# Optimization experiments

Measured on AMD Instinct MI355X. Metric: run time of the kernel, lower is better.

Reference implementation:

```python
import jax, jax.numpy as jnp
import numpy as np

D_MODEL = 256
HEADS = 4
HEAD_DIM = D_MODEL // HEADS  # 64
BN_EPS = 1e-5


def conv1(x, W, b):
    # Conv1d kernel_size=1 == per-position linear: x [B,C,N], W [O,C], b [O]
    return jnp.einsum('oc,bcn->bon', W, x) + b[:, None]


def setup_inputs() -> dict:
    key = jax.random.key(0)
    ks = jax.random.split(key, 12)
    B, N, M = 4, 4096, 4096
    s = 0.02
    return {
        'x': jax.random.normal(ks[0], (B, D_MODEL, N), jnp.float32),
        'source': jax.random.normal(ks[1], (B, D_MODEL, M), jnp.float32),
        'pq_w': jax.random.normal(ks[2], (D_MODEL, D_MODEL), jnp.float32) * s,
        'pq_b': jnp.zeros((D_MODEL,), jnp.float32),
        'pk_w': jax.random.normal(ks[3], (D_MODEL, D_MODEL), jnp.float32) * s,
        'pk_b': jnp.zeros((D_MODEL,), jnp.float32),
        'pv_w': jax.random.normal(ks[4], (D_MODEL, D_MODEL), jnp.float32) * s,
        'pv_b': jnp.zeros((D_MODEL,), jnp.float32),
        'merge_w': jax.random.normal(ks[5], (D_MODEL, D_MODEL), jnp.float32) * s,
        'merge_b': jnp.zeros((D_MODEL,), jnp.float32),
        'mlp1_w': jax.random.normal(ks[6], (2 * D_MODEL, 2 * D_MODEL), jnp.float32) * s,
        'mlp1_b': jax.random.normal(ks[7], (2 * D_MODEL,), jnp.float32) * s,
        'bn_gamma': jnp.ones((2 * D_MODEL,), jnp.float32),
        'bn_beta': jnp.zeros((2 * D_MODEL,), jnp.float32),
        'mlp2_w': jax.random.normal(ks[8], (D_MODEL, 2 * D_MODEL), jnp.float32) * s,
        'mlp2_b': jnp.zeros((D_MODEL,), jnp.float32),  # nn.init.constant_(mlp[-1].bias, 0.0)
    }


def reference(x, source, pq_w, pq_b, pk_w, pk_b, pv_w, pv_b,
              merge_w, merge_b, mlp1_w, mlp1_b, bn_gamma, bn_beta,
              mlp2_w, mlp2_b):
    B = x.shape[0]
    # projections; torch view(B, dim, heads, -1): channels split as (head_dim, heads)
    q = conv1(x, pq_w, pq_b).reshape(B, HEAD_DIM, HEADS, -1)       # [B,d,h,N]
    k = conv1(source, pk_w, pk_b).reshape(B, HEAD_DIM, HEADS, -1)  # [B,d,h,M]
    v = conv1(source, pv_w, pv_b).reshape(B, HEAD_DIM, HEADS, -1)
    scores = jnp.einsum('bdhn,bdhm->bhnm', q, k) / (HEAD_DIM ** 0.5)
    prob = jax.nn.softmax(scores, axis=-1)                          # [B,h,N,M]
    attn_out = jnp.einsum('bhnm,bdhm->bdhn', prob, v).reshape(B, D_MODEL, -1)
    message = conv1(attn_out, merge_w, merge_b)                     # [B,D,N]
    # MLP: conv(512->512) + BatchNorm1d (training-mode batch stats) + ReLU + conv(512->256)
    h = conv1(jnp.concatenate([x, message], axis=1), mlp1_w, mlp1_b)  # [B,2D,N]
    mean = jnp.mean(h, axis=(0, 2), keepdims=True)
    var = jnp.var(h, axis=(0, 2), keepdims=True)  # biased, as torch BN uses for normalization
    h = bn_gamma[:, None] * (h - mean) * jax.lax.rsqrt(var + BN_EPS) + bn_beta[:, None]
    h = jax.nn.relu(h)
    return conv1(h, mlp2_w, mlp2_b)
```

## Files before the change

kernel.cpp:

```cpp
#include <hip/hip_runtime.h>
#include <hip/hip_bf16.h>

#define D_MODEL 256
#define HEADS 4
#define HD 64
#define BATCH 4
#define SEQ 4096
#define NPOS (BATCH*SEQ)
#define SCALE_LOG2 0.18033688011112042f
#define MCHUNKS 2

typedef __attribute__((ext_vector_type(4))) float floatx4;
typedef __attribute__((ext_vector_type(8))) short bf16x8;
typedef __attribute__((ext_vector_type(4))) short bf16x4;
typedef __attribute__((ext_vector_type(4))) unsigned short ushortx4;

__device__ __forceinline__ float bf2f(unsigned short b) {
    return __uint_as_float(((unsigned int)b) << 16);
}
__device__ __forceinline__ unsigned short f2bf(float f) {
    unsigned int u = __float_as_uint(f);
    return (unsigned short)((u + 0x7fffu + ((u >> 16) & 1u)) >> 16);
}
__device__ __forceinline__ bf16x4 pack_bf16x4(float a, float b, float c, float d) {
    __hip_bfloat162 lo = __float22bfloat162_rn(float2{a, b});
    __hip_bfloat162 hi = __float22bfloat162_rn(float2{c, d});
    union { __hip_bfloat162 h2[2]; bf16x4 v; } u;
    u.h2[0] = lo; u.h2[1] = hi;
    return u.v;
}
__device__ __forceinline__ bf16x8 pack_bf16x8(floatx4 a, floatx4 b) {
    union { bf16x4 h[2]; bf16x8 v; } u;
    u.h[0] = pack_bf16x4(a[0], a[1], a[2], a[3]);
    u.h[1] = pack_bf16x4(b[0], b[1], b[2], b[3]);
    return u.v;
}
#define MFMA(a,b,c) __builtin_amdgcn_mfma_f32_16x16x32_bf16((a),(b),(c),0,0,0)
#define EXP2(x) __builtin_amdgcn_exp2f(x)

__global__ __launch_bounds__(256) void prep(
        const float* __restrict__ pq_w, const float* __restrict__ pk_w,
        const float* __restrict__ pv_w, const float* __restrict__ merge_w,
        const float* __restrict__ mlp1_w, const float* __restrict__ mlp2_w,
        const float* __restrict__ x, const float* __restrict__ src,
        unsigned short* __restrict__ wqb, unsigned short* __restrict__ wkb,
        unsigned short* __restrict__ wvb, unsigned short* __restrict__ wmt,
        unsigned short* __restrict__ w1b, unsigned short* __restrict__ w2b,
        unsigned short* __restrict__ xT, unsigned short* __restrict__ srcT)
{
    __shared__ unsigned short lT[64][264];
    const int t = threadIdx.x;
    const int bx = blockIdx.x;
    if (bx < 576) {
        int linear = bx * 1024 + t * 4;
        const float* srcW; unsigned short* dst; int off;
        if (linear < 65536)       { srcW = pq_w;   dst = wqb; off = 0; }
        else if (linear < 131072) { srcW = pk_w;   dst = wkb; off = 65536; }
        else if (linear < 196608) { srcW = pv_w;   dst = wvb; off = 131072; }
        else if (linear < 458752) { srcW = mlp1_w; dst = w1b; off = 196608; }
        else                      { srcW = mlp2_w; dst = w2b; off = 458752; }
        int i = linear - off;
        float4 w = *(const float4*)&srcW[i];
        ushortx4 s = { f2bf(w.x), f2bf(w.y), f2bf(w.z), f2bf(w.w) };
        *(ushortx4*)&dst[i] = s;
        return;
    }
    if (bx < 640) {
        int i = (bx - 576) * 1024 + t * 4;
        int cp = i >> 8, o = i & 255;
        int pc = ((cp & 63) << 2) | (cp >> 6);
        unsigned short s[4];
#pragma unroll
        for (int j = 0; j < 4; ++j)
            s[j] = f2bf(merge_w[(size_t)(o + j) * 256 + pc]);
        *(ushortx4*)&wmt[i] = *(const ushortx4*)s;
        return;
    }
    int z = bx - 640;
    const float* X = (z < 256) ? x : src;
    unsigned short* O = (z < 256) ? xT : srcT;
    int rem = z & 255;
    int b = rem >> 6, n0 = (rem & 63) * 64;
#pragma unroll
    for (int r = 0; r < 16; ++r) {
        int idx = r * 256 + t;
        int ch = idx >> 4, nnq = (idx & 15) * 4;
        float4 v4 = *(const float4*)&X[((size_t)b * 256 + ch) * SEQ + n0 + nnq];
        lT[nnq + 0][ch] = f2bf(v4.x);
        lT[nnq + 1][ch] = f2bf(v4.y);
        lT[nnq + 2][ch] = f2bf(v4.z);
        lT[nnq + 3][ch] = f2bf(v4.w);
    }
    __syncthreads();
#pragma unroll
    for (int r = 0; r < 8; ++r) {
        int idx = r * 256 + t;
        int row = idx >> 5, cg = (idx & 31) * 8;
        *(bf16x8*)&O[((size_t)b * SEQ + n0 + row) * 256 + cg] = *(const bf16x8*)&lT[row][cg];
    }
}

__global__ __launch_bounds__(256) void prep2(
        const float* __restrict__ mlp1_w, const float* __restrict__ mlp1_b,
        const float* __restrict__ merge_b, const unsigned short* __restrict__ wmt,
        unsigned short* __restrict__ w1f, float* __restrict__ b1f)
{
    __shared__ unsigned short lA[64][40];
    __shared__ unsigned short lB[128][40];
    const int t = threadIdx.x;
    if (blockIdx.y == 8) {
        int o2 = blockIdx.x * 256 + t;
        float s = mlp1_b[o2];
        for (int o = 0; o < 256; ++o)
            s += mlp1_w[(size_t)o2 * 512 + 256 + o] * merge_b[o];
        b1f[o2] = s;
        return;
    }
    const int lane = t & 63, wid = t >> 6;
    const int wm = wid >> 1, wn = wid & 1;
    const int lrow = lane & 15, quad = lane >> 4;
    const int o20 = blockIdx.y * 64;
    const int c0  = blockIdx.x * 128;

    floatx4 acc[2][4];
#pragma unroll
    for (int i = 0; i < 2; ++i)
#pragma unroll
        for (int j = 0; j < 4; ++j) acc[i][j] = (floatx4){0.f,0.f,0.f,0.f};

    for (int k0 = 0; k0 < 256; k0 += 32) {
#pragma unroll
        for (int r = 0; r < 2; ++r) {
            int linear = r * 1024 + t * 4;
            int row = linear >> 5, col = linear & 31;
            float4 w = *(const float4*)&mlp1_w[(size_t)(o20 + row) * 512 + 256 + k0 + col];
            ushortx4 s = { f2bf(w.x), f2bf(w.y), f2bf(w.z), f2bf(w.w) };
            *(ushortx4*)&lA[row][col] = s;
        }
#pragma unroll
        for (int r = 0; r < 2; ++r) {
            int linear = r * 256 + t;
            int row = linear >> 2, cg = (linear & 3) * 8;
            *(bf16x8*)&lB[row][cg] = *(const bf16x8*)&wmt[(size_t)(c0 + row) * 256 + k0 + cg];
        }
        __syncthreads();
        bf16x8 aF[2], bF[4];
        const int kq = quad * 8;
#pragma unroll
        for (int mt = 0; mt < 2; ++mt)
            aF[mt] = *(const bf16x8*)&lA[wm*32 + mt*16 + lrow][kq];
#pragma unroll
        for (int nt = 0; nt < 4; ++nt)
            bF[nt] = *(const bf16x8*)&lB[wn*64 + nt*16 + lrow][kq];
#pragma unroll
        for (int mt = 0; mt < 2; ++mt)
#pragma unroll
            for (int nt = 0; nt < 4; ++nt)
                acc[mt][nt] = MFMA(aF[mt], bF[nt], acc[mt][nt]);
        __syncthreads();
    }
#pragma unroll
    for (int nt = 0; nt < 4; ++nt) {
        int cp = c0 + wn*64 + nt*16 + lrow;
#pragma unroll
        for (int mt = 0; mt < 2; ++mt)
#pragma unroll
            for (int j = 0; j < 4; ++j) {
                int o2 = o20 + wm*32 + mt*16 + quad*4 + j;
                w1f[(size_t)o2 * 256 + cp] = f2bf(acc[mt][nt][j]);
            }
    }
}

__global__ __launch_bounds__(256) void proj_qkv_all(
        const unsigned short* __restrict__ Wq, const float* __restrict__ bq,
        const unsigned short* __restrict__ Wk, const float* __restrict__ bk,
        const unsigned short* __restrict__ Wv, const float* __restrict__ bv,
        const unsigned short* __restrict__ xT, const unsigned short* __restrict__ srcT,
        unsigned short* __restrict__ qo, unsigned short* __restrict__ ko,
        unsigned short* __restrict__ vo)
{
    __shared__ unsigned short smem[128 * 80];
    unsigned short (*lA)[40] = (unsigned short (*)[40])smem;
    unsigned short (*lB)[40] = (unsigned short (*)[40])(smem + 128 * 40);
    unsigned short (*stage)[72] = (unsigned short (*)[72])smem;
    unsigned short* stage2 = smem;
    const int t = threadIdx.x;
    const int lane = t & 63, wid = t >> 6;
    const int wm = wid >> 1, wn = wid & 1;
    const int lrow = lane & 15, quad = lane >> 4;
    const int mode = blockIdx.x >> 1;
    const int ob = (blockIdx.x & 1) * 128;
    const int n0 = blockIdx.y * 128;
    const int b  = blockIdx.z;
    const unsigned short* W  = (mode == 0) ? Wq : (mode == 1) ? Wk : Wv;
    const float* bias        = (mode == 0) ? bq : (mode == 1) ? bk : bv;
    const unsigned short* XT = (mode == 0) ? xT : srcT;
    unsigned short* out      = (mode == 0) ? qo : (mode == 1) ? ko : vo;

    const int srow[2] = { (0*256 + t) >> 2, (1*256 + t) >> 2 };
    const int scg = (t & 3) * 8;

    floatx4 acc[4][4];
#pragma unroll
    for (int i = 0; i < 4; ++i)
#pragma unroll
        for (int j = 0; j < 4; ++j) acc[i][j] = (floatx4){0.f,0.f,0.f,0.f};

    bf16x8 rW[2], rX[2];
#pragma unroll
    for (int r = 0; r < 2; ++r) {
        rW[r] = *(const bf16x8*)&W[(size_t)(ob + srow[r]) * 256 + scg];
        rX[r] = *(const bf16x8*)&XT[((size_t)b * SEQ + n0 + srow[r]) * 256 + scg];
    }
#pragma unroll
    for (int r = 0; r < 2; ++r) {
        *(bf16x8*)&lA[srow[r]][scg] = rW[r];
        *(bf16x8*)&lB[srow[r]][scg] = rX[r];
    }
    __syncthreads();

    for (int kc = 0; kc < 8; ++kc) {
        const bool pre = (kc + 1 < 8);
        if (pre) {
            const int k1 = (kc + 1) * 32;
#pragma unroll
            for (int r = 0; r < 2; ++r) {
                rW[r] = *(const bf16x8*)&W[(size_t)(ob + srow[r]) * 256 + k1 + scg];
                rX[r] = *(const bf16x8*)&XT[((size_t)b * SEQ + n0 + srow[r]) * 256 + k1 + scg];
            }
        }
        bf16x8 aF[4], bF[4];
        const int kq = quad * 8;
#pragma unroll
        for (int mt = 0; mt < 4; ++mt)
            aF[mt] = *(const bf16x8*)&lA[wm*64 + mt*16 + lrow][kq];
#pragma unroll
        for (int nt = 0; nt < 4; ++nt)
            bF[nt] = *(const bf16x8*)&lB[wn*64 + nt*16 + lrow][kq];
#pragma unroll
        for (int mt = 0; mt < 4; ++mt)
#pragma unroll
            for (int nt = 0; nt < 4; ++nt)
                acc[mt][nt] = MFMA(aF[mt], bF[nt], acc[mt][nt]);
        __syncthreads();
        if (pre) {
#pragma unroll
            for (int r = 0; r < 2; ++r) {
                *(bf16x8*)&lA[srow[r]][scg] = rW[r];
                *(bf16x8*)&lB[srow[r]][scg] = rX[r];
            }
            __syncthreads();
        }
    }
    const float osc = (mode == 0) ? SCALE_LOG2 : 1.0f;
    if (mode == 2) {
        for (int half = 0; half < 2; ++half) {
            __syncthreads();
            if (wm == half) {
#pragma unroll
                for (int mt = 0; mt < 4; ++mt)
#pragma unroll
                    for (int j = 0; j < 4; ++j) {
                        int ol = mt*16 + quad*4 + j;
                        float bvv = bias[ob + half*64 + ol];
#pragma unroll
                        for (int nt = 0; nt < 4; ++nt) {
                            int n = wn*64 + nt*16 + lrow;
                            stage2[ol*132 + n] = f2bf(acc[mt][nt][j] + bvv);
                        }
                    }
            }
            __syncthreads();
#pragma unroll
            for (int i = 0; i < 4; ++i) {
                int c = i * 256 + t;
                int row = c >> 4, sub = c & 15;
                int o = ob + half*64 + row;
                int d = o >> 2, h = o & 3;
                *(bf16x8*)&out[((size_t)(b*HEADS + h) * HD + d) * SEQ + n0 + sub*8] =
                    *(const bf16x8*)&stage2[row*132 + sub*8];
            }
        }
        return;
    }
    for (int half = 0; half < 2; ++half) {
        __syncthreads();
        if (wm == half) {
#pragma unroll
            for (int mt = 0; mt < 4; ++mt)
#pragma unroll
                for (int j = 0; j < 4; ++j) {
                    int o = ob + half*64 + mt*16 + quad*4 + j;
                    float bvv = bias[o];
                    int col = j*16 + mt*4 + quad;
#pragma unroll
                    for (int nt = 0; nt < 4; ++nt) {
                        int n = wn*64 + nt*16 + lrow;
                        stage[n][col] = f2bf((acc[mt][nt][j] + bvv) * osc);
                    }
                }
        }
        __syncthreads();
#pragma unroll
        for (int i = 0; i < 4; ++i) {
            int c = i * 256 + t;
            int n = c >> 3, h = (c >> 1) & 3, sub = c & 1;
            bf16x8 val = *(const bf16x8*)&stage[n][h*16 + sub*8];
            int d0 = (ob >> 2) + half*16 + sub*8;
            *(bf16x8*)&out[((size_t)(b*HEADS + h) * SEQ + n0 + n) * HD + d0] = val;
        }
    }
}

__global__ __launch_bounds__(256, 2) void flash_attn(
        const unsigned short* __restrict__ q,
        const unsigned short* __restrict__ k,
        const unsigned short* __restrict__ v,
        unsigned short* __restrict__ poO, float* __restrict__ pol)
{
    __shared__ unsigned short smem[2][9216];
    const int t = threadIdx.x, lane = t & 63, wid = t >> 6;
    const int lrow = lane & 15, quad = lane >> 4;
    const int bc = blockIdx.x, qt = blockIdx.y;
    const int bh = bc & 15, chunk = bc >> 4;
    const int hb = (bh & 3) * BATCH + (bh >> 2);
    const int r0 = qt * 256 + wid * 64;

    bf16x8 qf[4][2];
#pragma unroll
    for (int nh = 0; nh < 4; ++nh) {
        const size_t base = ((size_t)bh * SEQ + r0 + nh*16 + lrow) * HD;
        qf[nh][0] = *(const bf16x8*)&q[base + quad * 8];
        qf[nh][1] = *(const bf16x8*)&q[base + 32 + quad * 8];
    }
    bf16x8 ones;
#pragma unroll
    for (int i = 0; i < 8; ++i) ones[i] = (short)0x3F80;
    int mmv[2], cgv[2], krv[2];
#pragma unroll
    for (int r = 0; r < 2; ++r) {
        int linear = r * 256 + t;
        int mm = linear >> 3, cg = (linear & 7) * 8;
        int c2 = mm >> 5, mp = mm & 31;
        mmv[r] = mm; cgv[r] = cg;
        krv[r] = (c2 << 5) + ((mp & 4) << 2) + ((mp >> 3) << 2) + (mp & 3);
    }
    const size_t kbase = ((size_t)bh * SEQ + chunk * (SEQ/MCHUNKS));
    const size_t vbase = (size_t)bh * HD;
    const int moff = chunk * (SEQ/MCHUNKS);
    const int NIT = SEQ / MCHUNKS / 64;

    floatx4 oacc[4][4], oaccL[4];
#pragma unroll
    for (int nh = 0; nh < 4; ++nh) {
        oaccL[nh] = (floatx4){0.f,0.f,0.f,0.f};
#pragma unroll
        for (int i = 0; i < 4; ++i) oacc[nh][i] = (floatx4){0.f,0.f,0.f,0.f};
    }

    {
        bf16x8 pk[2], pv[2];
#pragma unroll
        for (int r = 0; r < 2; ++r) {
            pk[r] = *(const bf16x8*)&k[(kbase + mmv[r]) * HD + cgv[r]];
            pv[r] = *(const bf16x8*)&v[(vbase + mmv[r]) * SEQ + moff + cgv[r]];
        }
#pragma unroll
        for (int r = 0; r < 2; ++r) {
            *(bf16x8*)&smem[0][krv[r]*72 + cgv[r]]        = pk[r];
            *(bf16x8*)&smem[0][4608 + mmv[r]*72 + cgv[r]] = pv[r];
        }
    }
    __syncthreads();

    int p = 0;
#pragma unroll 1
    for (int it = 0; it < NIT; ++it) {
        bf16x8 pk[2], pv[2];
        const bool pre = (it + 1 < NIT);
        if (pre) {
            const int m1 = (it + 1) * 64;
#pragma unroll
            for (int r = 0; r < 2; ++r) {
                pk[r] = *(const bf16x8*)&k[(kbase + m1 + mmv[r]) * HD + cgv[r]];
                pv[r] = *(const bf16x8*)&v[(vbase + mmv[r]) * SEQ + moff + m1 + cgv[r]];
            }
        }
        const unsigned short* lS = smem[p];

#pragma unroll
        for (int c2 = 0; c2 < 2; ++c2) {
            floatx4 sa[2][4];
#pragma unroll
            for (int AB = 0; AB < 2; ++AB)
#pragma unroll
                for (int nh = 0; nh < 4; ++nh)
                    sa[AB][nh] = (floatx4){0.f,0.f,0.f,0.f};
            __builtin_amdgcn_s_setprio(1);
#pragma unroll
            for (int AB = 0; AB < 2; ++AB) {
#pragma unroll
                for (int kc = 0; kc < 2; ++kc) {
                    bf16x8 kf = *(const bf16x8*)&lS[(c2*32 + AB*16 + lrow)*72 + kc*32 + quad*8];
#pragma unroll
                    for (int nh = 0; nh < 4; ++nh)
                        sa[AB][nh] = MFMA(kf, qf[nh][kc], sa[AB][nh]);
                }
            }
            __builtin_amdgcn_s_setprio(0);
            bf16x8 pf8[4];
#pragma unroll
            for (int nh = 0; nh < 4; ++nh) {
                floatx4 ea, eb;
#pragma unroll
                for (int i = 0; i < 4; ++i) { ea[i] = EXP2(sa[0][nh][i]); eb[i] = EXP2(sa[1][nh][i]); }
                pf8[nh] = pack_bf16x8(ea, eb);
            }
            __builtin_amdgcn_s_setprio(1);
#pragma unroll
            for (int nh = 0; nh < 4; ++nh)
                oaccL[nh] = MFMA(ones, pf8[nh], oaccL[nh]);
#pragma unroll
            for (int dt = 0; dt < 4; ++dt) {
                bf16x8 vf = *(const bf16x8*)&lS[4608 + (dt*16 + lrow)*72 + c2*32 + quad*8];
#pragma unroll
                for (int nh = 0; nh < 4; ++nh)
                    oacc[nh][dt] = MFMA(vf, pf8[nh], oacc[nh][dt]);
            }
            __builtin_amdgcn_s_setprio(0);
        }
        if (pre) {
#pragma unroll
            for (int r = 0; r < 2; ++r) {
                *(bf16x8*)&smem[p^1][krv[r]*72 + cgv[r]]        = pk[r];
                *(bf16x8*)&smem[p^1][4608 + mmv[r]*72 + cgv[r]] = pv[r];
            }
        }
        __syncthreads();
        p ^= 1;
    }
    const size_t prow = (size_t)(chunk*16 + hb) * SEQ + qt * 256;
    if (lane < 16) {
#pragma unroll
        for (int nh = 0; nh < 4; ++nh)
            pol[prow + wid*64 + nh*16 + lrow] = oaccL[nh][0];
    }
    unsigned short* stB = (unsigned short*)&smem[0][0];
#pragma unroll
    for (int nh = 0; nh < 4; ++nh)
#pragma unroll
        for (int dt = 0; dt < 4; ++dt) {
            bf16x4 pv4 = pack_bf16x4(oacc[nh][dt][0], oacc[nh][dt][1],
                                     oacc[nh][dt][2], oacc[nh][dt][3]);
            *(bf16x4*)&stB[(wid*64 + nh*16 + lrow)*72 + dt*16 + quad*4] = pv4;
        }
    __syncthreads();
#pragma unroll
    for (int i = 0; i < 8; ++i) {
        int c = i * 256 + t;
        int row = c >> 3, sub = c & 7;
        *(bf16x8*)&poO[(prow + row) * HD + sub*8] = *(const bf16x8*)&stB[row*72 + sub*8];
    }
}

__global__ __launch_bounds__(256) void gemm_mlp1(
        const unsigned short* __restrict__ xT, const unsigned short* __restrict__ poO,
        const float* __restrict__ pol,
        const unsigned short* __restrict__ w1b, const unsigned short* __restrict__ w1f,
        const float* __restrict__ b1f, unsigned short* __restrict__ h1,
        float* __restrict__ sums, float* __restrict__ sumsq)
{
    __shared__ unsigned short lA[2][64][40];
    __shared__ unsigned short lB[2][128][40];
    __shared__ float sInv[256];
    const int t = threadIdx.x;
    const int lane = t & 63, wid = t >> 6;
    const int wm = wid >> 1, wn = wid & 1;
    const int lrow = lane & 15, quad = lane >> 4;
    const int o0 = blockIdx.x * 128;
    const int p0 = blockIdx.y * 64;
    const int b = p0 >> 12, n0 = p0 & (SEQ - 1);
    const size_t CH = (size_t)16 * SEQ * HD;

    {
        int h = t >> 6, nn = t & 63;
        int hb = h * BATCH + b;
        float l = 0.f;
#pragma unroll
        for (int c = 0; c < MCHUNKS; ++c)
            l += pol[((size_t)(c*16 + hb)) * SEQ + n0 + nn];
        sInv[t] = 1.0f / l;
    }
    __syncthreads();

    const int arow = t >> 2, acg = (t & 3) * 8;
    const int brow[2] = { (0*256 + t) >> 2, (1*256 + t) >> 2 };

    floatx4 acc[2][4];
#pragma unroll
    for (int i = 0; i < 2; ++i)
#pragma unroll
        for (int j = 0; j < 4; ++j) acc[i][j] = (floatx4){0.f,0.f,0.f,0.f};

    bf16x8 rA, rB[2];
    auto load_tile = [&](int k0) {
        if (k0 < 256) {
            rA = *(const bf16x8*)&xT[(size_t)(p0 + arow) * 256 + k0 + acg];
#pragma unroll
            for (int r = 0; r < 2; ++r)
                rB[r] = *(const bf16x8*)&w1b[(size_t)(o0 + brow[r]) * 512 + k0 + acg];
        } else {
            const int kk2 = k0 - 256;
            const int h = kk2 >> 6, d0 = kk2 & 63, hb = h * BATCH + b;
            const unsigned short* bse = &poO[((size_t)hb * SEQ + n0 + arow) * HD + d0 + acg];
            float inv = sInv[h*64 + arow];
            float fs[8];
#pragma unroll
            for (int i = 0; i < 8; ++i) fs[i] = 0.f;
#pragma unroll
            for (int c = 0; c < MCHUNKS; ++c) {
                bf16x8 a = *(const bf16x8*)(bse + (size_t)c * CH);
#pragma unroll
                for (int i = 0; i < 8; ++i)
                    fs[i] += bf2f((unsigned short)a[i]);
            }
            unsigned short res[8];
#pragma unroll
            for (int i = 0; i < 8; ++i)
                res[i] = f2bf(fs[i] * inv);
            rA = *(const bf16x8*)res;
#pragma unroll
            for (int r = 0; r < 2; ++r)
                rB[r] = *(const bf16x8*)&w1f[(size_t)(o0 + brow[r]) * 256 + kk2 + acg];
        }
    };

    load_tile(0);
    *(bf16x8*)&lA[0][arow][acg] = rA;
#pragma unroll
    for (int r = 0; r < 2; ++r) *(bf16x8*)&lB[0][brow[r]][acg] = rB[r];
    __syncthreads();

    int p = 0;
    for (int kc = 0; kc < 16; ++kc) {
        const bool pre = (kc + 1 < 16);
        if (pre) load_tile((kc + 1) * 32);
        bf16x8 aF[2], bF[4];
        const int kq = quad * 8;
#pragma unroll
        for (int mt = 0; mt < 2; ++mt)
            aF[mt] = *(const bf16x8*)&lA[p][wm*32 + mt*16 + lrow][kq];
#pragma unroll
        for (int nt = 0; nt < 4; ++nt)
            bF[nt] = *(const bf16x8*)&lB[p][wn*64 + nt*16 + lrow][kq];
#pragma unroll
        for (int mt = 0; mt < 2; ++mt)
#pragma unroll
            for (int nt = 0; nt < 4; ++nt)
                acc[mt][nt] = MFMA(aF[mt], bF[nt], acc[mt][nt]);
        if (pre) {
            *(bf16x8*)&lA[p^1][arow][acg] = rA;
#pragma unroll
            for (int r = 0; r < 2; ++r) *(bf16x8*)&lB[p^1][brow[r]][acg] = rB[r];
        }
        __syncthreads();
        p ^= 1;
    }
#pragma unroll
    for (int nt = 0; nt < 4; ++nt) {
        int o = o0 + wn*64 + nt*16 + lrow;
        float bvv = b1f[o];
        float s = 0.f, qs = 0.f;
#pragma unroll
        for (int mt = 0; mt < 2; ++mt)
#pragma unroll
            for (int j = 0; j < 4; ++j) {
                int pos = p0 + wm*32 + mt*16 + quad*4 + j;
                float val = acc[mt][nt][j] + bvv;
                h1[(size_t)pos * 512 + o] = f2bf(val);
                s += val; qs += val * val;
            }
        s  += __shfl_xor(s, 16);  s  += __shfl_xor(s, 32);
        qs += __shfl_xor(qs, 16); qs += __shfl_xor(qs, 32);
        if (lane < 16) {
            atomicAdd(&sums[o], s);
            atomicAdd(&sumsq[o], qs);
        }
    }
}

__global__ __launch_bounds__(256) void gemm_mlp2(
        const unsigned short* __restrict__ W2, const unsigned short* __restrict__ h1,
        const float* __restrict__ bias,
        const float* __restrict__ sums, const float* __restrict__ sumsq,
        const float* __restrict__ gamma, const float* __restrict__ beta,
        float* __restrict__ out)
{
    __shared__ unsigned short lA[2][128][40];
    __shared__ unsigned short lB[2][64][40];
    __shared__ float sSc[512], sSh[512];
    const int t = threadIdx.x;
    const int lane = t & 63, wid = t >> 6;
    const int wm = wid >> 1, wn = wid & 1;
    const int lrow = lane & 15, quad = lane >> 4;
    const int o0 = blockIdx.x * 128;
    const int p0 = blockIdx.y * 64;

#pragma unroll
    for (int cc = 0; cc < 2; ++cc) {
        int c = cc * 256 + t;
        float mean = sums[c] * (1.0f / NPOS);
        float var  = sumsq[c] * (1.0f / NPOS) - mean * mean;
        float sc = gamma[c] * rsqrtf(var + 1e-5f);
        sSc[c] = sc;
        sSh[c] = beta[c] - mean * sc;
    }
    __syncthreads();

    const int arow[2] = { (0*256 + t) >> 2, (1*256 + t) >> 2 };
    const int acg = (t & 3) * 8;
    const int brow = t >> 2;

    floatx4 acc[4][2];
#pragma unroll
    for (int i = 0; i < 4; ++i)
#pragma unroll
        for (int j = 0; j < 2; ++j) acc[i][j] = (floatx4){0.f,0.f,0.f,0.f};

    bf16x8 rW[2], rH;
    auto load_tile = [&](int k0) {
#pragma unroll
        for (int r = 0; r < 2; ++r)
            rW[r] = *(const bf16x8*)&W2[(size_t)(o0 + arow[r]) * 512 + k0 + acg];
        bf16x8 hv = *(const bf16x8*)&h1[(size_t)(p0 + brow) * 512 + k0 + acg];
        unsigned short res[8];
#pragma unroll
        for (int i = 0; i < 8; ++i) {
            int c = k0 + acg + i;
            float f = bf2f((unsigned short)hv[i]);
            f = fmaxf(f * sSc[c] + sSh[c], 0.f);
            res[i] = f2bf(f);
        }
        rH = *(const bf16x8*)res;
    };

    load_tile(0);
#pragma unroll
    for (int r = 0; r < 2; ++r) *(bf16x8*)&lA[0][arow[r]][acg] = rW[r];
    *(bf16x8*)&lB[0][brow][acg] = rH;
    __syncthreads();

    int p = 0;
    for (int kc = 0; kc < 16; ++kc) {
        const bool pre = (kc + 1 < 16);
        if (pre) load_tile((kc + 1) * 32);
        bf16x8 aF[4], bF[2];
        const int kq = quad * 8;
#pragma unroll
        for (int mt = 0; mt < 4; ++mt)
            aF[mt] = *(const bf16x8*)&lA[p][wm*64 + mt*16 + lrow][kq];
#pragma unroll
        for (int nt = 0; nt < 2; ++nt)
            bF[nt] = *(const bf16x8*)&lB[p][wn*32 + nt*16 + lrow][kq];
#pragma unroll
        for (int mt = 0; mt < 4; ++mt)
#pragma unroll
            for (int nt = 0; nt < 2; ++nt)
                acc[mt][nt] = MFMA(aF[mt], bF[nt], acc[mt][nt]);
        if (pre) {
#pragma unroll
            for (int r = 0; r < 2; ++r) *(bf16x8*)&lA[p^1][arow[r]][acg] = rW[r];
            *(bf16x8*)&lB[p^1][brow][acg] = rH;
        }
        __syncthreads();
        p ^= 1;
    }
#pragma unroll
    for (int mt = 0; mt < 4; ++mt)
#pragma unroll
        for (int j = 0; j < 4; ++j) {
            int o = o0 + wm*64 + mt*16 + quad*4 + j;
            float bvv = bias[o];
#pragma unroll
            for (int nt = 0; nt < 2; ++nt) {
                int pos = p0 + wn*32 + nt*16 + lrow;
                int b = pos >> 12, n = pos & (SEQ - 1);
                out[((size_t)b * D_MODEL + o) * SEQ + n] = acc[mt][nt][j] + bvv;
            }
        }
}

extern "C" void kernel_launch(void* const* d_in, const int* in_sizes, int n_in,
                              void* d_out, int out_size, void* d_ws, size_t ws_size,
                              hipStream_t stream)
{
    (void)in_sizes; (void)n_in; (void)out_size; (void)ws_size;
    const float* x        = (const float*)d_in[0];
    const float* source   = (const float*)d_in[1];
    const float* pq_w     = (const float*)d_in[2];
    const float* pq_b     = (const float*)d_in[3];
    const float* pk_w     = (const float*)d_in[4];
    const float* pk_b     = (const float*)d_in[5];
    const float* pv_w     = (const float*)d_in[6];
    const float* pv_b     = (const float*)d_in[7];
    const float* merge_w  = (const float*)d_in[8];
    const float* merge_b  = (const float*)d_in[9];
    const float* mlp1_w   = (const float*)d_in[10];
    const float* mlp1_b   = (const float*)d_in[11];
    const float* bn_gamma = (const float*)d_in[12];
    const float* bn_beta  = (const float*)d_in[13];
    const float* mlp2_w   = (const float*)d_in[14];
    const float* mlp2_b   = (const float*)d_in[15];
    float* out = (float*)d_out;

    char* ws = (char*)d_ws;
    const size_t MB = 1ull << 20;
    unsigned short* xT   = (unsigned short*)(ws);
    unsigned short* srcT = (unsigned short*)(ws + 8*MB);
    unsigned short* q    = (unsigned short*)(ws + 16*MB);
    unsigned short* kk   = (unsigned short*)(ws + 24*MB);
    unsigned short* v    = (unsigned short*)(ws + 32*MB);
    unsigned short* poO  = (unsigned short*)(ws + 40*MB);
    unsigned short* h1   = (unsigned short*)(ws + 16*MB);
    float* pol = (float*)(ws + 72*MB);
    unsigned short* wqb = (unsigned short*)(ws + 73*MB);
    unsigned short* wkb = wqb + 65536;
    unsigned short* wvb = wkb + 65536;
    unsigned short* wmt = wvb + 65536;
    unsigned short* w1b = wmt + 65536;
    unsigned short* w2b = w1b + 262144;
    unsigned short* w1f = w2b + 131072;
    float* b1f = (float*)(w1f + 131072);
    float* bn_sum = b1f + 512;
    float* bn_sumsq = bn_sum + 512;

    hipMemsetAsync(bn_sum, 0, 1024 * sizeof(float), stream);

    prep<<<dim3(1152), 256, 0, stream>>>(
        pq_w, pk_w, pv_w, merge_w, mlp1_w, mlp2_w, x, source,
        wqb, wkb, wvb, wmt, w1b, w2b, xT, srcT);
    prep2<<<dim3(2, 9), 256, 0, stream>>>(mlp1_w, mlp1_b, merge_b, wmt, w1f, b1f);
    proj_qkv_all<<<dim3(6, SEQ/128, BATCH), 256, 0, stream>>>(
        wqb, pq_b, wkb, pk_b, wvb, pv_b, xT, srcT, q, kk, v);
    flash_attn<<<dim3(16*MCHUNKS, SEQ/256), 256, 0, stream>>>(q, kk, v, poO, pol);
    gemm_mlp1<<<dim3(4, NPOS/64), 256, 0, stream>>>(
        xT, poO, pol, w1b, w1f, b1f, h1, bn_sum, bn_sumsq);
    gemm_mlp2<<<dim3(2, NPOS/64), 256, 0, stream>>>(
        w2b, h1, mlp2_b, bn_sum, bn_sumsq, bn_gamma, bn_beta, out);
}
```

Before: 253.8 us.

## Double-buffer QKV projection LDS and split attention combine into its own kernel

```diff
diff --git a/kernel.cpp b/kernel.cpp
--- a/kernel.cpp
+++ b/kernel.cpp
@@ -180,11 +180,9 @@
         unsigned short* __restrict__ qo, unsigned short* __restrict__ ko,
         unsigned short* __restrict__ vo)
 {
-    __shared__ unsigned short smem[128 * 80];
-    unsigned short (*lA)[40] = (unsigned short (*)[40])smem;
-    unsigned short (*lB)[40] = (unsigned short (*)[40])(smem + 128 * 40);
-    unsigned short (*stage)[72] = (unsigned short (*)[72])smem;
-    unsigned short* stage2 = smem;
+    __shared__ unsigned short smem[2][128 * 80];
+    unsigned short (*stage)[72] = (unsigned short (*)[72])&smem[0][0];
+    unsigned short* stage2 = &smem[0][0];
     const int t = threadIdx.x;
     const int lane = t & 63, wid = t >> 6;
     const int wm = wid >> 1, wn = wid & 1;
@@ -215,11 +213,12 @@
     }
 #pragma unroll
     for (int r = 0; r < 2; ++r) {
-        *(bf16x8*)&lA[srow[r]][scg] = rW[r];
-        *(bf16x8*)&lB[srow[r]][scg] = rX[r];
+        *(bf16x8*)&smem[0][srow[r]*40 + scg]           = rW[r];
+        *(bf16x8*)&smem[0][128*40 + srow[r]*40 + scg]  = rX[r];
     }
     __syncthreads();
 
+    int p = 0;
     for (int kc = 0; kc < 8; ++kc) {
         const bool pre = (kc + 1 < 8);
         if (pre) {
@@ -234,24 +233,24 @@
         const int kq = quad * 8;
 #pragma unroll
         for (int mt = 0; mt < 4; ++mt)
-            aF[mt] = *(const bf16x8*)&lA[wm*64 + mt*16 + lrow][kq];
+            aF[mt] = *(const bf16x8*)&smem[p][(wm*64 + mt*16 + lrow)*40 + kq];
 #pragma unroll
         for (int nt = 0; nt < 4; ++nt)
-            bF[nt] = *(const bf16x8*)&lB[wn*64 + nt*16 + lrow][kq];
+            bF[nt] = *(const bf16x8*)&smem[p][128*40 + (wn*64 + nt*16 + lrow)*40 + kq];
 #pragma unroll
         for (int mt = 0; mt < 4; ++mt)
 #pragma unroll
             for (int nt = 0; nt < 4; ++nt)
                 acc[mt][nt] = MFMA(aF[mt], bF[nt], acc[mt][nt]);
+        if (pre) {
+#pragma unroll
+            for (int r = 0; r < 2; ++r) {
+                *(bf16x8*)&smem[p^1][srow[r]*40 + scg]          = rW[r];
+                *(bf16x8*)&smem[p^1][128*40 + srow[r]*40 + scg] = rX[r];
+            }
+        }
         __syncthreads();
-        if (pre) {
-#pragma unroll
-            for (int r = 0; r < 2; ++r) {
-                *(bf16x8*)&lA[srow[r]][scg] = rW[r];
-                *(bf16x8*)&lB[srow[r]][scg] = rX[r];
-            }
-            __syncthreads();
-        }
+        p ^= 1;
     }
     const float osc = (mode == 0) ? SCALE_LOG2 : 1.0f;
     if (mode == 2) {
@@ -464,35 +463,50 @@
     }
 }
 
+__global__ __launch_bounds__(256) void combine_o(
+        const unsigned short* __restrict__ poO, const float* __restrict__ pol,
+        unsigned short* __restrict__ attnC)
+{
+    const int t = threadIdx.x;
+    const int p0 = blockIdx.x * 32;
+    const size_t CH = (size_t)16 * SEQ * HD;
+#pragma unroll
+    for (int i = 0; i < 4; ++i) {
+        int g = i * 256 + t;
+        int pl = g >> 5;
+        int cg = (g & 31) * 8;
+        int pos = p0 + pl;
+        int b = pos >> 12, n = pos & (SEQ - 1);
+        int h = cg >> 6, d0 = cg & 63;
+        int hb = h * BATCH + b;
+        const unsigned short* bse = &poO[((size_t)hb * SEQ + n) * HD + d0];
+        float l0 = pol[(size_t)hb * SEQ + n];
+        float l1 = pol[(size_t)(16 + hb) * SEQ + n];
+        float inv = 1.0f / (l0 + l1);
+        bf16x8 a0 = *(const bf16x8*)bse;
+        bf16x8 a1 = *(const bf16x8*)(bse + CH);
+        unsigned short res[8];
+#pragma unroll
+        for (int j = 0; j < 8; ++j)
+            res[j] = f2bf((bf2f((unsigned short)a0[j]) + bf2f((unsigned short)a1[j])) * inv);
+        *(bf16x8*)&attnC[(size_t)pos * 256 + cg] = *(const bf16x8*)res;
+    }
+}
+
 __global__ __launch_bounds__(256) void gemm_mlp1(
-        const unsigned short* __restrict__ xT, const unsigned short* __restrict__ poO,
-        const float* __restrict__ pol,
+        const unsigned short* __restrict__ xT, const unsigned short* __restrict__ attnC,
         const unsigned short* __restrict__ w1b, const unsigned short* __restrict__ w1f,
         const float* __restrict__ b1f, unsigned short* __restrict__ h1,
         float* __restrict__ sums, float* __restrict__ sumsq)
 {
     __shared__ unsigned short lA[2][64][40];
     __shared__ unsigned short lB[2][128][40];
-    __shared__ float sInv[256];
     const int t = threadIdx.x;
     const int lane = t & 63, wid = t >> 6;
     const int wm = wid >> 1, wn = wid & 1;
     const int lrow = lane & 15, quad = lane >> 4;
     const int o0 = blockIdx.x * 128;
     const int p0 = blockIdx.y * 64;
-    const int b = p0 >> 12, n0 = p0 & (SEQ - 1);
-    const size_t CH = (size_t)16 * SEQ * HD;
-
-    {
-        int h = t >> 6, nn = t & 63;
-        int hb = h * BATCH + b;
-        float l = 0.f;
-#pragma unroll
-        for (int c = 0; c < MCHUNKS; ++c)
-            l += pol[((size_t)(c*16 + hb)) * SEQ + n0 + nn];
-        sInv[t] = 1.0f / l;
-    }
-    __syncthreads();
 
     const int arow = t >> 2, acg = (t & 3) * 8;
     const int brow[2] = { (0*256 + t) >> 2, (1*256 + t) >> 2 };
@@ -512,24 +526,7 @@
                 rB[r] = *(const bf16x8*)&w1b[(size_t)(o0 + brow[r]) * 512 + k0 + acg];
         } else {
             const int kk2 = k0 - 256;
-            const int h = kk2 >> 6, d0 = kk2 & 63, hb = h * BATCH + b;
-            const unsigned short* bse = &poO[((size_t)hb * SEQ + n0 + arow) * HD + d0 + acg];
-            float inv = sInv[h*64 + arow];
-            float fs[8];
-#pragma unroll
-            for (int i = 0; i < 8; ++i) fs[i] = 0.f;
-#pragma unroll
-            for (int c = 0; c < MCHUNKS; ++c) {
-                bf16x8 a = *(const bf16x8*)(bse + (size_t)c * CH);
-#pragma unroll
-                for (int i = 0; i < 8; ++i)
-                    fs[i] += bf2f((unsigned short)a[i]);
-            }
-            unsigned short res[8];
-#pragma unroll
-            for (int i = 0; i < 8; ++i)
-                res[i] = f2bf(fs[i] * inv);
-            rA = *(const bf16x8*)res;
+            rA = *(const bf16x8*)&attnC[(size_t)(p0 + arow) * 256 + kk2 + acg];
 #pragma unroll
             for (int r = 0; r < 2; ++r)
                 rB[r] = *(const bf16x8*)&w1f[(size_t)(o0 + brow[r]) * 256 + kk2 + acg];
@@ -722,6 +719,7 @@
     unsigned short* kk   = (unsigned short*)(ws + 24*MB);
     unsigned short* v    = (unsigned short*)(ws + 32*MB);
     unsigned short* poO  = (unsigned short*)(ws + 40*MB);
+    unsigned short* attnC= (unsigned short*)(ws + 56*MB);
     unsigned short* h1   = (unsigned short*)(ws + 16*MB);
     float* pol = (float*)(ws + 72*MB);
     unsigned short* wqb = (unsigned short*)(ws + 73*MB);
@@ -744,8 +742,9 @@
     proj_qkv_all<<<dim3(6, SEQ/128, BATCH), 256, 0, stream>>>(
         wqb, pq_b, wkb, pk_b, wvb, pv_b, xT, srcT, q, kk, v);
     flash_attn<<<dim3(16*MCHUNKS, SEQ/256), 256, 0, stream>>>(q, kk, v, poO, pol);
+    combine_o<<<dim3(NPOS/32), 256, 0, stream>>>(poO, pol, attnC);
     gemm_mlp1<<<dim3(4, NPOS/64), 256, 0, stream>>>(
-        xT, poO, pol, w1b, w1f, b1f, h1, bn_sum, bn_sumsq);
+        xT, attnC, w1b, w1f, b1f, h1, bn_sum, bn_sumsq);
     gemm_mlp2<<<dim3(2, NPOS/64), 256, 0, stream>>>(
         w2b, h1, mlp2_b, bn_sum, bn_sumsq, bn_gamma, bn_beta, out);
 }
```

After: 256.5 us. About the same (+1.1%).

## Merge prep kernels and memset into one launch, double-buffer QKV projection LDS

Applied to the files above, without the earlier changes.

```diff
diff --git a/kernel.cpp b/kernel.cpp
--- a/kernel.cpp
+++ b/kernel.cpp
@@ -38,17 +38,20 @@
 #define MFMA(a,b,c) __builtin_amdgcn_mfma_f32_16x16x32_bf16((a),(b),(c),0,0,0)
 #define EXP2(x) __builtin_amdgcn_exp2f(x)
 
-__global__ __launch_bounds__(256) void prep(
+__global__ __launch_bounds__(256) void prep_all(
         const float* __restrict__ pq_w, const float* __restrict__ pk_w,
         const float* __restrict__ pv_w, const float* __restrict__ merge_w,
         const float* __restrict__ mlp1_w, const float* __restrict__ mlp2_w,
+        const float* __restrict__ mlp1_b, const float* __restrict__ merge_b,
         const float* __restrict__ x, const float* __restrict__ src,
         unsigned short* __restrict__ wqb, unsigned short* __restrict__ wkb,
-        unsigned short* __restrict__ wvb, unsigned short* __restrict__ wmt,
+        unsigned short* __restrict__ wvb,
         unsigned short* __restrict__ w1b, unsigned short* __restrict__ w2b,
-        unsigned short* __restrict__ xT, unsigned short* __restrict__ srcT)
+        unsigned short* __restrict__ xT, unsigned short* __restrict__ srcT,
+        unsigned short* __restrict__ w1f, float* __restrict__ b1f,
+        float* __restrict__ bn_zero)
 {
-    __shared__ unsigned short lT[64][264];
+    __shared__ unsigned short smem[64 * 264];
     const int t = threadIdx.x;
     const int bx = blockIdx.x;
     if (bx < 576) {
@@ -65,111 +68,107 @@
         *(ushortx4*)&dst[i] = s;
         return;
     }
-    if (bx < 640) {
-        int i = (bx - 576) * 1024 + t * 4;
-        int cp = i >> 8, o = i & 255;
-        int pc = ((cp & 63) << 2) | (cp >> 6);
-        unsigned short s[4];
-#pragma unroll
-        for (int j = 0; j < 4; ++j)
-            s[j] = f2bf(merge_w[(size_t)(o + j) * 256 + pc]);
-        *(ushortx4*)&wmt[i] = *(const ushortx4*)s;
+    if (bx < 1088) {
+        unsigned short (*lT)[264] = (unsigned short (*)[264])smem;
+        int z = bx - 576;
+        const float* X = (z < 256) ? x : src;
+        unsigned short* O = (z < 256) ? xT : srcT;
+        int rem = z & 255;
+        int b = rem >> 6, n0 = (rem & 63) * 64;
+#pragma unroll
+        for (int r = 0; r < 16; ++r) {
+            int idx = r * 256 + t;
+            int ch = idx >> 4, nnq = (idx & 15) * 4;
+            float4 v4 = *(const float4*)&X[((size_t)b * 256 + ch) * SEQ + n0 + nnq];
+            lT[nnq + 0][ch] = f2bf(v4.x);
+            lT[nnq + 1][ch] = f2bf(v4.y);
+            lT[nnq + 2][ch] = f2bf(v4.z);
+            lT[nnq + 3][ch] = f2bf(v4.w);
+        }
+        __syncthreads();
+#pragma unroll
+        for (int r = 0; r < 8; ++r) {
+            int idx = r * 256 + t;
+            int row = idx >> 5, cg = (idx & 31) * 8;
+            *(bf16x8*)&O[((size_t)b * SEQ + n0 + row) * 256 + cg] = *(const bf16x8*)&lT[row][cg];
+        }
         return;
     }
-    int z = bx - 640;
-    const float* X = (z < 256) ? x : src;
-    unsigned short* O = (z < 256) ? xT : srcT;
-    int rem = z & 255;
-    int b = rem >> 6, n0 = (rem & 63) * 64;
-#pragma unroll
-    for (int r = 0; r < 16; ++r) {
-        int idx = r * 256 + t;
-        int ch = idx >> 4, nnq = (idx & 15) * 4;
-        float4 v4 = *(const float4*)&X[((size_t)b * 256 + ch) * SEQ + n0 + nnq];
-        lT[nnq + 0][ch] = f2bf(v4.x);
-        lT[nnq + 1][ch] = f2bf(v4.y);
-        lT[nnq + 2][ch] = f2bf(v4.z);
-        lT[nnq + 3][ch] = f2bf(v4.w);
-    }
-    __syncthreads();
-#pragma unroll
-    for (int r = 0; r < 8; ++r) {
-        int idx = r * 256 + t;
-        int row = idx >> 5, cg = (idx & 31) * 8;
-        *(bf16x8*)&O[((size_t)b * SEQ + n0 + row) * 256 + cg] = *(const bf16x8*)&lT[row][cg];
-    }
-}
-
-__global__ __launch_bounds__(256) void prep2(
-        const float* __restrict__ mlp1_w, const float* __restrict__ mlp1_b,
-        const float* __restrict__ merge_b, const unsigned short* __restrict__ wmt,
-        unsigned short* __restrict__ w1f, float* __restrict__ b1f)
-{
-    __shared__ unsigned short lA[64][40];
-    __shared__ unsigned short lB[128][40];
-    const int t = threadIdx.x;
-    if (blockIdx.y == 8) {
-        int o2 = blockIdx.x * 256 + t;
+    if (bx < 1104) {
+        unsigned short (*lA)[40] = (unsigned short (*)[40])smem;
+        unsigned short (*lB)[40] = (unsigned short (*)[40])(smem + 64 * 40);
+        const int lane = t & 63, wid = t >> 6;
+        const int wm = wid >> 1, wn = wid & 1;
+        const int lrow = lane & 15, quad = lane >> 4;
+        const int fb = bx - 1088;
+        const int c0  = (fb & 1) * 128;
+        const int o20 = (fb >> 1) * 64;
+
+        floatx4 acc[2][4];
+#pragma unroll
+        for (int i = 0; i < 2; ++i)
+#pragma unroll
+            for (int j = 0; j < 4; ++j) acc[i][j] = (floatx4){0.f,0.f,0.f,0.f};
+
+        for (int k0 = 0; k0 < 256; k0 += 32) {
+#pragma unroll
+            for (int r = 0; r < 2; ++r) {
+                int linear = r * 1024 + t * 4;
+                int row = linear >> 5, col = linear & 31;
+                float4 w = *(const float4*)&mlp1_w[(size_t)(o20 + row) * 512 + 256 + k0 + col];
+                ushortx4 s = { f2bf(w.x), f2bf(w.y), f2bf(w.z), f2bf(w.w) };
+                *(ushortx4*)&lA[row][col] = s;
+            }
+#pragma unroll
+            for (int r = 0; r < 2; ++r) {
+                int linear = r * 256 + t;
+                int row = linear >> 2, cg = (linear & 3) * 8;
+                int cp = c0 + row;
+                int pc = ((cp & 63) << 2) | (cp >> 6);
+                unsigned short s[8];
+#pragma unroll
+                for (int j = 0; j < 8; ++j)
+                    s[j] = f2bf(merge_w[(size_t)(k0 + cg + j) * 256 + pc]);
+                *(bf16x8*)&lB[row][cg] = *(const bf16x8*)s;
+            }
+            __syncthreads();
+            bf16x8 aF[2], bF[4];
+            const int kq = quad * 8;
+#pragma unroll
+            for (int mt = 0; mt < 2; ++mt)
+                aF[mt] = *(const bf16x8*)&lA[wm*32 + mt*16 + lrow][kq];
+#pragma unroll
+            for (int nt = 0; nt < 4; ++nt)
+                bF[nt] = *(const bf16x8*)&lB[wn*64 + nt*16 + lrow][kq];
+#pragma unroll
+            for (int mt = 0; mt < 2; ++mt)
+#pragma unroll
+                for (int nt = 0; nt < 4; ++nt)
+                    acc[mt][nt] = MFMA(aF[mt], bF[nt], acc[mt][nt]);
+            __syncthreads();
+        }
+#pragma unroll
+        for (int nt = 0; nt < 4; ++nt) {
+            int cp = c0 + wn*64 + nt*16 + lrow;
+#pragma unroll
+            for (int mt = 0; mt < 2; ++mt)
+#pragma unroll
+                for (int j = 0; j < 4; ++j) {
+                    int o2 = o20 + wm*32 + mt*16 + quad*4 + j;
+                    w1f[(size_t)o2 * 256 + cp] = f2bf(acc[mt][nt][j]);
+                }
+        }
+        return;
+    }
+    if (bx < 1106) {
+        int o2 = (bx - 1104) * 256 + t;
         float s = mlp1_b[o2];
         for (int o = 0; o < 256; ++o)
             s += mlp1_w[(size_t)o2 * 512 + 256 + o] * merge_b[o];
         b1f[o2] = s;
         return;
     }
-    const int lane = t & 63, wid = t >> 6;
-    const int wm = wid >> 1, wn = wid & 1;
-    const int lrow = lane & 15, quad = lane >> 4;
-    const int o20 = blockIdx.y * 64;
-    const int c0  = blockIdx.x * 128;
-
-    floatx4 acc[2][4];
-#pragma unroll
-    for (int i = 0; i < 2; ++i)
-#pragma unroll
-        for (int j = 0; j < 4; ++j) acc[i][j] = (floatx4){0.f,0.f,0.f,0.f};
-
-    for (int k0 = 0; k0 < 256; k0 += 32) {
-#pragma unroll
-        for (int r = 0; r < 2; ++r) {
-            int linear = r * 1024 + t * 4;
-            int row = linear >> 5, col = linear & 31;
-            float4 w = *(const float4*)&mlp1_w[(size_t)(o20 + row) * 512 + 256 + k0 + col];
-            ushortx4 s = { f2bf(w.x), f2bf(w.y), f2bf(w.z), f2bf(w.w) };
-            *(ushortx4*)&lA[row][col] = s;
-        }
-#pragma unroll
-        for (int r = 0; r < 2; ++r) {
-            int linear = r * 256 + t;
-            int row = linear >> 2, cg = (linear & 3) * 8;
-            *(bf16x8*)&lB[row][cg] = *(const bf16x8*)&wmt[(size_t)(c0 + row) * 256 + k0 + cg];
-        }
-        __syncthreads();
-        bf16x8 aF[2], bF[4];
-        const int kq = quad * 8;
-#pragma unroll
-        for (int mt = 0; mt < 2; ++mt)
-            aF[mt] = *(const bf16x8*)&lA[wm*32 + mt*16 + lrow][kq];
-#pragma unroll
-        for (int nt = 0; nt < 4; ++nt)
-            bF[nt] = *(const bf16x8*)&lB[wn*64 + nt*16 + lrow][kq];
-#pragma unroll
-        for (int mt = 0; mt < 2; ++mt)
-#pragma unroll
-            for (int nt = 0; nt < 4; ++nt)
-                acc[mt][nt] = MFMA(aF[mt], bF[nt], acc[mt][nt]);
-        __syncthreads();
-    }
-#pragma unroll
-    for (int nt = 0; nt < 4; ++nt) {
-        int cp = c0 + wn*64 + nt*16 + lrow;
-#pragma unroll
-        for (int mt = 0; mt < 2; ++mt)
-#pragma unroll
-            for (int j = 0; j < 4; ++j) {
-                int o2 = o20 + wm*32 + mt*16 + quad*4 + j;
-                w1f[(size_t)o2 * 256 + cp] = f2bf(acc[mt][nt][j]);
-            }
-    }
+    *(float4*)&bn_zero[t * 4] = float4{0.f, 0.f, 0.f, 0.f};
 }
 
 __global__ __launch_bounds__(256) void proj_qkv_all(
@@ -180,11 +179,9 @@
         unsigned short* __restrict__ qo, unsigned short* __restrict__ ko,
         unsigned short* __restrict__ vo)
 {
-    __shared__ unsigned short smem[128 * 80];
-    unsigned short (*lA)[40] = (unsigned short (*)[40])smem;
-    unsigned short (*lB)[40] = (unsigned short (*)[40])(smem + 128 * 40);
-    unsigned short (*stage)[72] = (unsigned short (*)[72])smem;
-    unsigned short* stage2 = smem;
+    __shared__ unsigned short smem[2][128 * 80];
+    unsigned short (*stage)[72] = (unsigned short (*)[72])&smem[0][0];
+    unsigned short* stage2 = &smem[0][0];
     const int t = threadIdx.x;
     const int lane = t & 63, wid = t >> 6;
     const int wm = wid >> 1, wn = wid & 1;
@@ -215,11 +212,12 @@
     }
 #pragma unroll
     for (int r = 0; r < 2; ++r) {
-        *(bf16x8*)&lA[srow[r]][scg] = rW[r];
-        *(bf16x8*)&lB[srow[r]][scg] = rX[r];
+        *(bf16x8*)&smem[0][srow[r]*40 + scg]           = rW[r];
+        *(bf16x8*)&smem[0][128*40 + srow[r]*40 + scg]  = rX[r];
     }
     __syncthreads();
 
+    int p = 0;
     for (int kc = 0; kc < 8; ++kc) {
         const bool pre = (kc + 1 < 8);
         if (pre) {
@@ -234,24 +232,24 @@
         const int kq = quad * 8;
 #pragma unroll
         for (int mt = 0; mt < 4; ++mt)
-            aF[mt] = *(const bf16x8*)&lA[wm*64 + mt*16 + lrow][kq];
+            aF[mt] = *(const bf16x8*)&smem[p][(wm*64 + mt*16 + lrow)*40 + kq];
 #pragma unroll
         for (int nt = 0; nt < 4; ++nt)
-            bF[nt] = *(const bf16x8*)&lB[wn*64 + nt*16 + lrow][kq];
+            bF[nt] = *(const bf16x8*)&smem[p][128*40 + (wn*64 + nt*16 + lrow)*40 + kq];
 #pragma unroll
         for (int mt = 0; mt < 4; ++mt)
 #pragma unroll
             for (int nt = 0; nt < 4; ++nt)
                 acc[mt][nt] = MFMA(aF[mt], bF[nt], acc[mt][nt]);
+        if (pre) {
+#pragma unroll
+            for (int r = 0; r < 2; ++r) {
+                *(bf16x8*)&smem[p^1][srow[r]*40 + scg]          = rW[r];
+                *(bf16x8*)&smem[p^1][128*40 + srow[r]*40 + scg] = rX[r];
+            }
+        }
         __syncthreads();
-        if (pre) {
-#pragma unroll
-            for (int r = 0; r < 2; ++r) {
-                *(bf16x8*)&lA[srow[r]][scg] = rW[r];
-                *(bf16x8*)&lB[srow[r]][scg] = rX[r];
-            }
-            __syncthreads();
-        }
+        p ^= 1;
     }
     const float osc = (mode == 0) ? SCALE_LOG2 : 1.0f;
     if (mode == 2) {
@@ -727,20 +725,16 @@
     unsigned short* wqb = (unsigned short*)(ws + 73*MB);
     unsigned short* wkb = wqb + 65536;
     unsigned short* wvb = wkb + 65536;
-    unsigned short* wmt = wvb + 65536;
-    unsigned short* w1b = wmt + 65536;
+    unsigned short* w1b = wvb + 65536;
     unsigned short* w2b = w1b + 262144;
     unsigned short* w1f = w2b + 131072;
     float* b1f = (float*)(w1f + 131072);
     float* bn_sum = b1f + 512;
     float* bn_sumsq = bn_sum + 512;
 
-    hipMemsetAsync(bn_sum, 0, 1024 * sizeof(float), stream);
-
-    prep<<<dim3(1152), 256, 0, stream>>>(
-        pq_w, pk_w, pv_w, merge_w, mlp1_w, mlp2_w, x, source,
-        wqb, wkb, wvb, wmt, w1b, w2b, xT, srcT);
-    prep2<<<dim3(2, 9), 256, 0, stream>>>(mlp1_w, mlp1_b, merge_b, wmt, w1f, b1f);
+    prep_all<<<dim3(1107), 256, 0, stream>>>(
+        pq_w, pk_w, pv_w, merge_w, mlp1_w, mlp2_w, mlp1_b, merge_b, x, source,
+        wqb, wkb, wvb, w1b, w2b, xT, srcT, w1f, b1f, bn_sum);
     proj_qkv_all<<<dim3(6, SEQ/128, BATCH), 256, 0, stream>>>(
         wqb, pq_b, wkb, pk_b, wvb, pv_b, xT, srcT, q, kk, v);
     flash_attn<<<dim3(16*MCHUNKS, SEQ/256), 256, 0, stream>>>(q, kk, v, poO, pol);
```

New measurement: 243.4 us. -4.1%, faster.
